# Kernel optimization log

Hardware: AMD Instinct MI355X
Metric: run time of the kernel (lower is better)

## Reference

```python
import jax, jax.numpy as jnp
import numpy as np

DEPTH = 9            # perfect binary tree depth (root=level 0, leaves=level DEPTH)
N_TREES = 128
H = 256              # h_size == x_size (ndata['h'] init uses x_size)
NPT = 2 ** (DEPTH + 1) - 1   # 1023 nodes per tree
N = N_TREES * NPT            # 130944 total nodes


def _levels():
    """Static per-level (node, left-child, right-child) global index arrays."""
    base = np.arange(N_TREES, dtype=np.int64)[:, None] * NPT
    out = []
    for l in range(DEPTH + 1):
        loc = np.arange(2 ** l - 1, 2 ** (l + 1) - 1, dtype=np.int64)
        nodes = (base + loc[None, :]).reshape(-1)
        if l < DEPTH:
            cl = (base + (2 * loc + 1)[None, :]).reshape(-1)
            cr = (base + (2 * loc + 2)[None, :]).reshape(-1)
        else:
            cl = cr = None
        out.append((jnp.asarray(nodes),
                    None if cl is None else jnp.asarray(cl),
                    None if cr is None else jnp.asarray(cr)))
    return out


def setup_inputs() -> dict:
    key = jax.random.key(0)
    ks = jax.random.split(key, 10)
    s = lambda d: 1.0 / np.sqrt(d)
    return {
        "wordid": jax.random.randint(ks[0], (N,), 0, 32000),
        "mask":   jax.random.randint(ks[1], (N,), 0, 2),
        "emb":    jax.random.normal(ks[2], (32000, H), jnp.float32) * 0.02,
        "W_iou":  jax.random.normal(ks[3], (H, 3 * H), jnp.float32) * s(H),
        "U_iou":  jax.random.normal(ks[4], (2 * H, 3 * H), jnp.float32) * s(2 * H),
        "U_f_w":  jax.random.normal(ks[5], (2 * H, 2 * H), jnp.float32) * s(2 * H),
        "U_f_b":  jax.random.normal(ks[6], (2 * H,), jnp.float32) * 0.01,
        "b_iou":  jax.random.normal(ks[7], (3 * H,), jnp.float32) * 0.01,
        "lin_w":  jax.random.normal(ks[8], (H, 4), jnp.float32) * s(H),
        "lin_b":  jax.random.normal(ks[9], (4,), jnp.float32) * 0.01,
    }


def _apply_node(iou, b_iou, c_in, mh_in):
    i, o, u = jnp.split(iou + b_iou, 3, axis=1)
    i, o, u = jax.nn.sigmoid(i), jax.nn.sigmoid(o), jnp.tanh(u)
    c = i * u + c_in
    h = o * jnp.tanh(c)
    return h, c, jnp.maximum(h, mh_in)


def reference(wordid, mask, emb, W_iou, U_iou, U_f_w, U_f_b, b_iou, lin_w, lin_b):
    levels = _levels()
    x = emb[wordid * mask]                                  # [N, H]
    iou0 = (x @ W_iou) * mask[:, None].astype(x.dtype)      # leaf/pre-set iou [N, 3H]

    h = jnp.zeros((N, H), x.dtype)
    c = jnp.zeros((N, H), x.dtype)
    mh = jnp.zeros((N, H), x.dtype)

    # leaves: no incoming messages -> apply with preset iou, c=0, max_h=0
    li, _, _ = levels[DEPTH]
    hh, cc, mm = _apply_node(iou0[li], b_iou, 0.0, 0.0)
    h, c, mh = h.at[li].set(hh), c.at[li].set(cc), mh.at[li].set(mm)

    # internal levels, bottom-up (DGL prop_nodes_topo)
    for l in range(DEPTH - 1, -1, -1):
        ni, cl, cr = levels[l]
        h_cat = jnp.concatenate([h[cl], h[cr]], axis=1)     # [M, 2H]
        f = jax.nn.sigmoid(h_cat @ U_f_w + U_f_b)           # [M, 2H]
        fl, fr = jnp.split(f, 2, axis=1)
        c_red = fl * c[cl] + fr * c[cr]
        mh_red = jnp.maximum(mh[cl], mh[cr])
        iou = h_cat @ U_iou                                  # overwrites preset iou
        hh, cc, mm = _apply_node(iou, b_iou, c_red, mh_red)
        h, c, mh = h.at[ni].set(hh), c.at[ni].set(cc), mh.at[ni].set(mm)

    return (h + mh) @ lin_w + lin_b                         # logits [N, num_classes]
```

## Files before the change

kernel.cpp:

```cpp
#include <hip/hip_runtime.h>
#include <hip/hip_bf16.h>


#define NTREES 128
#define NPT    1023
#define HS     256

typedef __hip_bfloat16 bf16;
typedef unsigned short us8 __attribute__((ext_vector_type(8)));
typedef short bf16x8 __attribute__((ext_vector_type(8)));
typedef float f32x4 __attribute__((ext_vector_type(4)));

typedef __attribute__((address_space(1))) const void gvoid;
typedef __attribute__((address_space(3))) void svoid;
#define GLD16(gp, lp) \
    __builtin_amdgcn_global_load_lds((gvoid*)(gp), (svoid*)(lp), 16, 0, 0)

__device__ __forceinline__ float bits2f(unsigned short b) {
    return __uint_as_float(((unsigned)b) << 16);
}
__device__ __forceinline__ float ld_bf(const bf16* p) {
    return bits2f(*reinterpret_cast<const unsigned short*>(p));
}
__device__ __forceinline__ unsigned short f2bits(float x) {
    bf16 h = __float2bfloat16(x);
    return *reinterpret_cast<unsigned short*>(&h);
}
__device__ __forceinline__ float sigm(float x) { return 1.0f / (1.0f + expf(-x)); }

#define WT_ELEMS (768 * 256)
#define UT_ELEMS (1280 * 512)

__global__ __launch_bounds__(256) void prep_w(
    const float* __restrict__ W_iou, const float* __restrict__ U_f_w,
    const float* __restrict__ U_iou, bf16* __restrict__ Wt, bf16* __restrict__ Ut)
{
    const int i = blockIdx.x * 256 + threadIdx.x;
    if (i < WT_ELEMS) {
        const int n = i >> 8, k = i & 255;
        Wt[i] = __float2bfloat16(W_iou[k * 768 + n]);
    } else if (i < WT_ELEMS + UT_ELEMS) {
        const int j = i - WT_ELEMS;
        const int n = j >> 9, k = j & 511;
        const float v = (n < 512) ? U_f_w[k * 512 + n] : U_iou[k * 768 + (n - 512)];
        Ut[j] = __float2bfloat16(v);
    }
}

__global__ __launch_bounds__(256) void leaf_gemm_mfma(
    const int* __restrict__ wordid, const int* __restrict__ mask,
    const float* __restrict__ emb, const bf16* __restrict__ Wt,
    bf16* __restrict__ lin, const int g0)
{
    __shared__ __align__(16) short a_s[128 * 32];
    __shared__ __align__(16) short b_s[128 * 32];
    const int t    = threadIdx.x;
    const int bm0  = blockIdx.x * 128;
    const int bn0  = blockIdx.y * 128;
    const int lane = t & 63, wave = t >> 6;

    const int arow_lo = t >> 2;
    const int k8t     = (t & 3) * 8;
    const float* aptr[2];
    int amask[2];
    #pragma unroll
    for (int p = 0; p < 2; ++p) {
        const int row  = p * 64 + arow_lo;
        const int gr   = g0 + bm0 + row;
        const int tree = gr >> 9, idx = gr & 511;
        const int node = tree * NPT + 511 + idx;
        amask[p] = mask[node];
        aptr[p]  = emb + (long)wordid[node] * HS + k8t;
    }

    const int l4a = lane >> 2;
    const int k8  = (lane & 3) * 8;
    const bf16* bSrc[2];
    #pragma unroll
    for (int q = 0; q < 2; ++q) {
        const int n = wave * 2 + q;
        bSrc[q] = Wt + (long)(bn0 + n * 16 + l4a) * 256 + k8;
    }

    const int wr = wave >> 1, wc = wave & 1;
    const int fr = lane & 15, l4 = lane >> 4;

    f32x4 acc[4][4];
    #pragma unroll
    for (int i = 0; i < 4; ++i)
        #pragma unroll
        for (int j = 0; j < 4; ++j) acc[i][j] = (f32x4){0.f, 0.f, 0.f, 0.f};

    for (int kt = 0; kt < 256; kt += 32) {
        __syncthreads();
        #pragma unroll
        for (int q = 0; q < 2; ++q)
            GLD16(bSrc[q] + kt, &b_s[(wave * 2 + q) * 512]);
        #pragma unroll
        for (int p = 0; p < 2; ++p) {
            short tmp[8];
            if (amask[p]) {
                const float4 v0 = *(const float4*)(aptr[p] + kt);
                const float4 v1 = *(const float4*)(aptr[p] + kt + 4);
                tmp[0] = (short)f2bits(v0.x); tmp[1] = (short)f2bits(v0.y);
                tmp[2] = (short)f2bits(v0.z); tmp[3] = (short)f2bits(v0.w);
                tmp[4] = (short)f2bits(v1.x); tmp[5] = (short)f2bits(v1.y);
                tmp[6] = (short)f2bits(v1.z); tmp[7] = (short)f2bits(v1.w);
            } else {
                #pragma unroll
                for (int q = 0; q < 8; ++q) tmp[q] = 0;
            }
            *(us8*)&a_s[p * 2048 + t * 8] = *(us8*)&tmp[0];
        }
        __syncthreads();
        bf16x8 af[4], bg[4];
        #pragma unroll
        for (int i = 0; i < 4; ++i)
            af[i] = *(const bf16x8*)&a_s[(wr * 64 + i * 16 + fr) * 32 + l4 * 8];
        #pragma unroll
        for (int j = 0; j < 4; ++j)
            bg[j] = *(const bf16x8*)&b_s[(wc * 64 + j * 16 + fr) * 32 + l4 * 8];
        #pragma unroll
        for (int i = 0; i < 4; ++i)
            #pragma unroll
            for (int j = 0; j < 4; ++j)
                acc[i][j] = __builtin_amdgcn_mfma_f32_16x16x32_bf16(
                    af[i], bg[j], acc[i][j], 0, 0, 0);
    }
    #pragma unroll
    for (int i = 0; i < 4; ++i) {
        const int row0 = bm0 + wr * 64 + i * 16 + l4 * 4;
        #pragma unroll
        for (int j = 0; j < 4; ++j) {
            const int col = bn0 + wc * 64 + j * 16 + fr;
            #pragma unroll
            for (int q = 0; q < 4; ++q)
                lin[(long)(row0 + q) * 768 + col] = __float2bfloat16(acc[i][j][q]);
        }
    }
}

__global__ __launch_bounds__(256) void level_gemm_mfma(
    const bf16* __restrict__ h_child, const bf16* __restrict__ Ut,
    bf16* __restrict__ lin, const int lvl, const int p0, const int M)
{
    __shared__ __align__(16) short a_s[128 * 32];
    __shared__ __align__(16) short b_s[128 * 32];
    const int t    = threadIdx.x;
    const int bm0  = blockIdx.x * 128;
    const int bn0  = blockIdx.y * 128;
    const int lane = t & 63, wave = t >> 6;

    const int l4a = lane >> 2;
    const int k8  = (lane & 3) * 8;
    const bf16* aSrc[2];
    const bf16* bSrc[2];
    #pragma unroll
    for (int q = 0; q < 2; ++q) {
        const int n = wave * 2 + q;
        int p = p0 + bm0 + n * 16 + l4a;
        if (p >= M) p = M - 1;
        const int tl  = p >> lvl;
        const int idx = p & ((1 << lvl) - 1);
        const int cls = tl * (2 << lvl) + 2 * idx;
        aSrc[q] = h_child + (long)cls * HS + k8;
        bSrc[q] = Ut + (long)(bn0 + n * 16 + l4a) * 512 + k8;
    }

    const int wr = wave >> 1, wc = wave & 1;
    const int fr = lane & 15, l4 = lane >> 4;

    f32x4 acc[4][4];
    #pragma unroll
    for (int i = 0; i < 4; ++i)
        #pragma unroll
        for (int j = 0; j < 4; ++j) acc[i][j] = (f32x4){0.f, 0.f, 0.f, 0.f};

    for (int kt = 0; kt < 512; kt += 32) {
        __syncthreads();
        #pragma unroll
        for (int q = 0; q < 2; ++q) {
            GLD16(aSrc[q] + kt, &a_s[(wave * 2 + q) * 512]);
            GLD16(bSrc[q] + kt, &b_s[(wave * 2 + q) * 512]);
        }
        __syncthreads();
        bf16x8 af[4], bg[4];
        #pragma unroll
        for (int i = 0; i < 4; ++i)
            af[i] = *(const bf16x8*)&a_s[(wr * 64 + i * 16 + fr) * 32 + l4 * 8];
        #pragma unroll
        for (int j = 0; j < 4; ++j)
            bg[j] = *(const bf16x8*)&b_s[(wc * 64 + j * 16 + fr) * 32 + l4 * 8];
        #pragma unroll
        for (int i = 0; i < 4; ++i)
            #pragma unroll
            for (int j = 0; j < 4; ++j)
                acc[i][j] = __builtin_amdgcn_mfma_f32_16x16x32_bf16(
                    af[i], bg[j], acc[i][j], 0, 0, 0);
    }
    #pragma unroll
    for (int i = 0; i < 4; ++i) {
        const int row0 = bm0 + wr * 64 + i * 16 + l4 * 4;
        #pragma unroll
        for (int j = 0; j < 4; ++j) {
            const int col = bn0 + wc * 64 + j * 16 + fr;
            #pragma unroll
            for (int q = 0; q < 4; ++q) {
                const int rr = row0 + q;
                if (p0 + rr < M)
                    lin[(long)rr * 1280 + col] = __float2bfloat16(acc[i][j][q]);
            }
        }
    }
}

__device__ __forceinline__ void logits_reduce(
    float s, const float* __restrict__ lin_w, const float* __restrict__ lin_b,
    float* __restrict__ outp, int j)
{
    const float4 w = *(const float4*)(lin_w + j * 4);
    float p0 = s * w.x, p1 = s * w.y, p2 = s * w.z, p3 = s * w.w;
    #pragma unroll
    for (int off = 32; off > 0; off >>= 1) {
        p0 += __shfl_down(p0, off);
        p1 += __shfl_down(p1, off);
        p2 += __shfl_down(p2, off);
        p3 += __shfl_down(p3, off);
    }
    __shared__ float red[4][4];
    const int w_id = j >> 6, lane = j & 63;
    if (lane == 0) { red[w_id][0] = p0; red[w_id][1] = p1; red[w_id][2] = p2; red[w_id][3] = p3; }
    __syncthreads();
    if (j < 4) {
        outp[j] = red[0][j] + red[1][j] + red[2][j] + red[3][j] + lin_b[j];
    }
}

__global__ __launch_bounds__(256) void leaf_epi(
    const int* __restrict__ mask, const bf16* __restrict__ lin,
    const float* __restrict__ b_iou,
    const float* __restrict__ lin_w, const float* __restrict__ lin_b,
    bf16* __restrict__ h_s, bf16* __restrict__ c_s, bf16* __restrict__ mh_s,
    float* __restrict__ out, const int g0, const int s0)
{
    const int rc   = blockIdx.x;
    const int gr   = g0 + rc;
    const int tree = gr >> 9, idx = gr & 511;
    const int node = tree * NPT + 511 + idx;
    const int j    = threadIdx.x;
    const int m    = mask[node];
    const bf16* lr = lin + (long)rc * 768;

    const float pi = (m ? ld_bf(lr + j)       : 0.0f) + b_iou[j];
    const float po = (m ? ld_bf(lr + 256 + j) : 0.0f) + b_iou[256 + j];
    const float pu = (m ? ld_bf(lr + 512 + j) : 0.0f) + b_iou[512 + j];
    const float iv = sigm(pi), ov = sigm(po), uv = tanhf(pu);
    const float cv  = iv * uv;
    const float hv  = ov * tanhf(cv);
    const float mhv = fmaxf(hv, 0.0f);

    const long o = (long)(s0 + rc) * HS + j;
    h_s[o]  = __float2bfloat16(hv);
    c_s[o]  = __float2bfloat16(cv);
    mh_s[o] = __float2bfloat16(mhv);

    logits_reduce(hv + mhv, lin_w, lin_b, out + (long)node * 4, j);
}

__global__ __launch_bounds__(256) void level_epi(
    const bf16* __restrict__ lin,
    const float* __restrict__ b_iou, const float* __restrict__ U_f_b,
    const float* __restrict__ lin_w, const float* __restrict__ lin_b,
    const bf16* __restrict__ c_c, const bf16* __restrict__ mh_c,
    bf16* __restrict__ h_p, bf16* __restrict__ c_p, bf16* __restrict__ mh_p,
    float* __restrict__ out, const int lvl, const int p0, const int tree0)
{
    const int rc   = blockIdx.x;
    const int p    = p0 + rc;
    const int tl   = p >> lvl, idx = p & ((1 << lvl) - 1);
    const int node = (tree0 + tl) * NPT + (1 << lvl) - 1 + idx;
    const int cls  = tl * (2 << lvl) + 2 * idx;
    const int j    = threadIdx.x;
    const bf16* lr = lin + (long)rc * 1280;

    const float fl = sigm(ld_bf(lr + j)       + U_f_b[j]);
    const float fr = sigm(ld_bf(lr + 256 + j) + U_f_b[256 + j]);
    const float pi = ld_bf(lr + 512 + j)  + b_iou[j];
    const float po = ld_bf(lr + 768 + j)  + b_iou[256 + j];
    const float pu = ld_bf(lr + 1024 + j) + b_iou[512 + j];

    const float ccl = ld_bf(c_c  + (long)cls * HS + j);
    const float ccr = ld_bf(c_c  + (long)(cls + 1) * HS + j);
    const float mhl = ld_bf(mh_c + (long)cls * HS + j);
    const float mhr = ld_bf(mh_c + (long)(cls + 1) * HS + j);

    const float c_red  = fl * ccl + fr * ccr;
    const float mh_red = fmaxf(mhl, mhr);

    const float iv = sigm(pi), ov = sigm(po), uv = tanhf(pu);
    const float cv  = iv * uv + c_red;
    const float hv  = ov * tanhf(cv);
    const float mhv = fmaxf(hv, mh_red);

    const long o = (long)p * HS + j;
    h_p[o]  = __float2bfloat16(hv);
    c_p[o]  = __float2bfloat16(cv);
    mh_p[o] = __float2bfloat16(mhv);

    logits_reduce(hv + mhv, lin_w, lin_b, out + (long)node * 4, j);
}

extern "C" void kernel_launch(void* const* d_in, const int* in_sizes, int n_in,
                              void* d_out, int out_size, void* d_ws, size_t ws_size,
                              hipStream_t stream) {
    const int*   wordid = (const int*)d_in[0];
    const int*   mask   = (const int*)d_in[1];
    const float* emb    = (const float*)d_in[2];
    const float* W_iou  = (const float*)d_in[3];
    const float* U_iou  = (const float*)d_in[4];
    const float* U_f_w  = (const float*)d_in[5];
    const float* U_f_b  = (const float*)d_in[6];
    const float* b_iou  = (const float*)d_in[7];
    const float* lin_w  = (const float*)d_in[8];
    const float* lin_b  = (const float*)d_in[9];
    float* out = (float*)d_out;

    const size_t wElems   = (size_t)WT_ELEMS + UT_ELEMS;
    const size_t ws_elems = ws_size / 2;
    auto baseElems = [&](int T) -> size_t {
        return wElems + (size_t)T * 589824;
    };
    const size_t minLin = 128 * 1280;
    int T = 8;
    const int cands[4] = {128, 64, 32, 16};
    for (int ci = 0; ci < 4; ++ci) {
        if (baseElems(cands[ci]) + minLin <= ws_elems) { T = cands[ci]; break; }
    }
    const size_t linCap = ws_elems - baseElems(T);

    bf16* Wt = (bf16*)d_ws;
    bf16* Ut = Wt + WT_ELEMS;
    const size_t aR = (size_t)T * 512 * HS;
    const size_t bR = (size_t)T * 256 * HS;
    bf16* hA  = Ut  + UT_ELEMS;
    bf16* cA  = hA  + aR;
    bf16* mhA = cA  + aR;
    bf16* hB  = mhA + aR;
    bf16* cB  = hB  + bR;
    bf16* mhB = cB  + bR;
    bf16* lin = mhB + bR;

    prep_w<<<(int)((wElems + 255) / 256), 256, 0, stream>>>(
        W_iou, U_f_w, U_iou, Wt, Ut);

    int CRl = (int)((linCap / 768) & ~(size_t)127);
    int CRv = (int)((linCap / 1280) & ~(size_t)127);
    if (CRl < 128) CRl = 128;
    if (CRv < 128) CRv = 128;

    for (int tree0 = 0; tree0 < NTREES; tree0 += T) {
        const int Ml = T * 512;
        for (int r0 = 0; r0 < Ml; r0 += CRl) {
            const int rows = (Ml - r0) < CRl ? (Ml - r0) : CRl;
            const int g0   = tree0 * 512 + r0;
            leaf_gemm_mfma<<<dim3(rows / 128, 6), 256, 0, stream>>>(
                wordid, mask, emb, Wt, lin, g0);
            leaf_epi<<<rows, 256, 0, stream>>>(
                mask, lin, b_iou, lin_w, lin_b, hA, cA, mhA, out, g0, r0);
        }
        bool childIsA = true;
        for (int l = 8; l >= 0; --l) {
            bf16 *hc, *cc, *mc, *hp, *cp, *mp;
            if (childIsA) { hc = hA; cc = cA; mc = mhA; hp = hB; cp = cB; mp = mhB; }
            else          { hc = hB; cc = cB; mc = mhB; hp = hA; cp = cA; mp = mhA; }
            const int M = T << l;
            for (int p0 = 0; p0 < M; p0 += CRv) {
                const int rows = (M - p0) < CRv ? (M - p0) : CRv;
                level_gemm_mfma<<<dim3((rows + 127) / 128, 10), 256, 0, stream>>>(
                    hc, Ut, lin, l, p0, M);
                level_epi<<<rows, 256, 0, stream>>>(
                    lin, b_iou, U_f_b, lin_w, lin_b, cc, mc, hp, cp, mp,
                    out, l, p0, tree0);
            }
            childIsA = !childIsA;
        }
    }
}
```

Baseline: 522.9 us.

## Map one wavefront per node row in epilogues with vectorized loads and fast math

The leaf and level epilogue kernels now assign one 64-lane wavefront per row, not one 256-thread block. Each lane handles four columns with 8-byte vector loads and stores, and the logits reduction becomes a wave-level xor shuffle, dropping the shared-memory stage and the block barrier. Sigmoid and tanh are rewritten with fast exp and hardware reciprocal. The aim is fewer blocks, wider memory accesses and no synchronisation, at some cost in transcendental accuracy.

Result: faster. 461.1 us (-11.8%).

```diff
diff --git a/kernel.cpp b/kernel.cpp
--- a/kernel.cpp
+++ b/kernel.cpp
@@ -8,6 +8,7 @@
 
 typedef __hip_bfloat16 bf16;
 typedef unsigned short us8 __attribute__((ext_vector_type(8)));
+typedef unsigned short us4 __attribute__((ext_vector_type(4)));
 typedef short bf16x8 __attribute__((ext_vector_type(8)));
 typedef float f32x4 __attribute__((ext_vector_type(4)));
 
@@ -19,14 +20,16 @@
 __device__ __forceinline__ float bits2f(unsigned short b) {
     return __uint_as_float(((unsigned)b) << 16);
 }
-__device__ __forceinline__ float ld_bf(const bf16* p) {
-    return bits2f(*reinterpret_cast<const unsigned short*>(p));
-}
 __device__ __forceinline__ unsigned short f2bits(float x) {
     bf16 h = __float2bfloat16(x);
     return *reinterpret_cast<unsigned short*>(&h);
 }
-__device__ __forceinline__ float sigm(float x) { return 1.0f / (1.0f + expf(-x)); }
+__device__ __forceinline__ float fsigm(float x) {
+    return __builtin_amdgcn_rcpf(1.0f + __expf(-x));
+}
+__device__ __forceinline__ float ftanh(float x) {
+    return 1.0f - 2.0f * __builtin_amdgcn_rcpf(1.0f + __expf(2.0f * x));
+}
 
 #define WT_ELEMS (768 * 256)
 #define UT_ELEMS (1280 * 512)
@@ -214,57 +217,62 @@
     }
 }
 
-__device__ __forceinline__ void logits_reduce(
-    float s, const float* __restrict__ lin_w, const float* __restrict__ lin_b,
-    float* __restrict__ outp, int j)
-{
-    const float4 w = *(const float4*)(lin_w + j * 4);
-    float p0 = s * w.x, p1 = s * w.y, p2 = s * w.z, p3 = s * w.w;
-    #pragma unroll
-    for (int off = 32; off > 0; off >>= 1) {
-        p0 += __shfl_down(p0, off);
-        p1 += __shfl_down(p1, off);
-        p2 += __shfl_down(p2, off);
-        p3 += __shfl_down(p3, off);
-    }
-    __shared__ float red[4][4];
-    const int w_id = j >> 6, lane = j & 63;
-    if (lane == 0) { red[w_id][0] = p0; red[w_id][1] = p1; red[w_id][2] = p2; red[w_id][3] = p3; }
-    __syncthreads();
-    if (j < 4) {
-        outp[j] = red[0][j] + red[1][j] + red[2][j] + red[3][j] + lin_b[j];
-    }
-}
-
 __global__ __launch_bounds__(256) void leaf_epi(
     const int* __restrict__ mask, const bf16* __restrict__ lin,
     const float* __restrict__ b_iou,
     const float* __restrict__ lin_w, const float* __restrict__ lin_b,
     bf16* __restrict__ h_s, bf16* __restrict__ c_s, bf16* __restrict__ mh_s,
-    float* __restrict__ out, const int g0, const int s0)
+    float* __restrict__ out, const int g0, const int s0, const int rows)
 {
-    const int rc   = blockIdx.x;
+    const int wave = threadIdx.x >> 6, lane = threadIdx.x & 63;
+    const int rc   = blockIdx.x * 4 + wave;
+    if (rc >= rows) return;
     const int gr   = g0 + rc;
     const int tree = gr >> 9, idx = gr & 511;
     const int node = tree * NPT + 511 + idx;
-    const int j    = threadIdx.x;
-    const int m    = mask[node];
-    const bf16* lr = lin + (long)rc * 768;
-
-    const float pi = (m ? ld_bf(lr + j)       : 0.0f) + b_iou[j];
-    const float po = (m ? ld_bf(lr + 256 + j) : 0.0f) + b_iou[256 + j];
-    const float pu = (m ? ld_bf(lr + 512 + j) : 0.0f) + b_iou[512 + j];
-    const float iv = sigm(pi), ov = sigm(po), uv = tanhf(pu);
-    const float cv  = iv * uv;
-    const float hv  = ov * tanhf(cv);
-    const float mhv = fmaxf(hv, 0.0f);
-
-    const long o = (long)(s0 + rc) * HS + j;
-    h_s[o]  = __float2bfloat16(hv);
-    c_s[o]  = __float2bfloat16(cv);
-    mh_s[o] = __float2bfloat16(mhv);
-
-    logits_reduce(hv + mhv, lin_w, lin_b, out + (long)node * 4, j);
+    const float msk = mask[node] ? 1.0f : 0.0f;
+    const int j0   = lane * 4;
+
+    const bf16* lr = lin + (long)rc * 768 + j0;
+    const us4 vi = *(const us4*)(lr);
+    const us4 vo = *(const us4*)(lr + 256);
+    const us4 vu = *(const us4*)(lr + 512);
+    const float4 bi = *(const float4*)(b_iou + j0);
+    const float4 bo = *(const float4*)(b_iou + 256 + j0);
+    const float4 bu = *(const float4*)(b_iou + 512 + j0);
+
+    us4 sh, sc, sm;
+    float p0 = 0.f, p1 = 0.f, p2 = 0.f, p3 = 0.f;
+    #pragma unroll
+    for (int q = 0; q < 4; ++q) {
+        const float pi = msk * bits2f(vi[q]) + ((const float*)&bi)[q];
+        const float po = msk * bits2f(vo[q]) + ((const float*)&bo)[q];
+        const float pu = msk * bits2f(vu[q]) + ((const float*)&bu)[q];
+        const float iv = fsigm(pi), ov = fsigm(po), uv = ftanh(pu);
+        const float cv  = iv * uv;
+        const float hv  = ov * ftanh(cv);
+        const float mhv = fmaxf(hv, 0.0f);
+        sh[q] = f2bits(hv); sc[q] = f2bits(cv); sm[q] = f2bits(mhv);
+        const float s = hv + mhv;
+        const float4 w = *(const float4*)(lin_w + (j0 + q) * 4);
+        p0 += s * w.x; p1 += s * w.y; p2 += s * w.z; p3 += s * w.w;
+    }
+    const long o = (long)(s0 + rc) * HS + j0;
+    *(us4*)(h_s + o)  = sh;
+    *(us4*)(c_s + o)  = sc;
+    *(us4*)(mh_s + o) = sm;
+
+    #pragma unroll
+    for (int m = 1; m < 64; m <<= 1) {
+        p0 += __shfl_xor(p0, m); p1 += __shfl_xor(p1, m);
+        p2 += __shfl_xor(p2, m); p3 += __shfl_xor(p3, m);
+    }
+    if (lane == 0) {
+        float4 r;
+        r.x = p0 + lin_b[0]; r.y = p1 + lin_b[1];
+        r.z = p2 + lin_b[2]; r.w = p3 + lin_b[3];
+        *(float4*)(out + (long)node * 4) = r;
+    }
 }
 
 __global__ __launch_bounds__(256) void level_epi(
@@ -273,41 +281,70 @@
     const float* __restrict__ lin_w, const float* __restrict__ lin_b,
     const bf16* __restrict__ c_c, const bf16* __restrict__ mh_c,
     bf16* __restrict__ h_p, bf16* __restrict__ c_p, bf16* __restrict__ mh_p,
-    float* __restrict__ out, const int lvl, const int p0, const int tree0)
+    float* __restrict__ out, const int lvl, const int p0r, const int tree0,
+    const int rows)
 {
-    const int rc   = blockIdx.x;
-    const int p    = p0 + rc;
+    const int wave = threadIdx.x >> 6, lane = threadIdx.x & 63;
+    const int rc   = blockIdx.x * 4 + wave;
+    if (rc >= rows) return;
+    const int p    = p0r + rc;
     const int tl   = p >> lvl, idx = p & ((1 << lvl) - 1);
     const int node = (tree0 + tl) * NPT + (1 << lvl) - 1 + idx;
     const int cls  = tl * (2 << lvl) + 2 * idx;
-    const int j    = threadIdx.x;
-    const bf16* lr = lin + (long)rc * 1280;
-
-    const float fl = sigm(ld_bf(lr + j)       + U_f_b[j]);
-    const float fr = sigm(ld_bf(lr + 256 + j) + U_f_b[256 + j]);
-    const float pi = ld_bf(lr + 512 + j)  + b_iou[j];
-    const float po = ld_bf(lr + 768 + j)  + b_iou[256 + j];
-    const float pu = ld_bf(lr + 1024 + j) + b_iou[512 + j];
-
-    const float ccl = ld_bf(c_c  + (long)cls * HS + j);
-    const float ccr = ld_bf(c_c  + (long)(cls + 1) * HS + j);
-    const float mhl = ld_bf(mh_c + (long)cls * HS + j);
-    const float mhr = ld_bf(mh_c + (long)(cls + 1) * HS + j);
-
-    const float c_red  = fl * ccl + fr * ccr;
-    const float mh_red = fmaxf(mhl, mhr);
-
-    const float iv = sigm(pi), ov = sigm(po), uv = tanhf(pu);
-    const float cv  = iv * uv + c_red;
-    const float hv  = ov * tanhf(cv);
-    const float mhv = fmaxf(hv, mh_red);
-
-    const long o = (long)p * HS + j;
-    h_p[o]  = __float2bfloat16(hv);
-    c_p[o]  = __float2bfloat16(cv);
-    mh_p[o] = __float2bfloat16(mhv);
-
-    logits_reduce(hv + mhv, lin_w, lin_b, out + (long)node * 4, j);
+    const int j0   = lane * 4;
+
+    const bf16* lr = lin + (long)rc * 1280 + j0;
+    const us4 vfl = *(const us4*)(lr);
+    const us4 vfr = *(const us4*)(lr + 256);
+    const us4 vi  = *(const us4*)(lr + 512);
+    const us4 vo  = *(const us4*)(lr + 768);
+    const us4 vu  = *(const us4*)(lr + 1024);
+    const us4 vcl = *(const us4*)(c_c  + (long)cls * HS + j0);
+    const us4 vcr = *(const us4*)(c_c  + (long)(cls + 1) * HS + j0);
+    const us4 vml = *(const us4*)(mh_c + (long)cls * HS + j0);
+    const us4 vmr = *(const us4*)(mh_c + (long)(cls + 1) * HS + j0);
+    const float4 ufl = *(const float4*)(U_f_b + j0);
+    const float4 ufr = *(const float4*)(U_f_b + 256 + j0);
+    const float4 bi  = *(const float4*)(b_iou + j0);
+    const float4 bo  = *(const float4*)(b_iou + 256 + j0);
+    const float4 bu  = *(const float4*)(b_iou + 512 + j0);
+
+    us4 sh, sc, sm;
+    float p0 = 0.f, p1 = 0.f, p2 = 0.f, p3 = 0.f;
+    #pragma unroll
+    for (int q = 0; q < 4; ++q) {
+        const float fl = fsigm(bits2f(vfl[q]) + ((const float*)&ufl)[q]);
+        const float fr = fsigm(bits2f(vfr[q]) + ((const float*)&ufr)[q]);
+        const float pi = bits2f(vi[q]) + ((const float*)&bi)[q];
+        const float po = bits2f(vo[q]) + ((const float*)&bo)[q];
+        const float pu = bits2f(vu[q]) + ((const float*)&bu)[q];
+        const float c_red  = fl * bits2f(vcl[q]) + fr * bits2f(vcr[q]);
+        const float mh_red = fmaxf(bits2f(vml[q]), bits2f(vmr[q]));
+        const float iv = fsigm(pi), ov = fsigm(po), uv = ftanh(pu);
+        const float cv  = iv * uv + c_red;
+        const float hv  = ov * ftanh(cv);
+        const float mhv = fmaxf(hv, mh_red);
+        sh[q] = f2bits(hv); sc[q] = f2bits(cv); sm[q] = f2bits(mhv);
+        const float s = hv + mhv;
+        const float4 w = *(const float4*)(lin_w + (j0 + q) * 4);
+        p0 += s * w.x; p1 += s * w.y; p2 += s * w.z; p3 += s * w.w;
+    }
+    const long o = (long)p * HS + j0;
+    *(us4*)(h_p + o)  = sh;
+    *(us4*)(c_p + o)  = sc;
+    *(us4*)(mh_p + o) = sm;
+
+    #pragma unroll
+    for (int m = 1; m < 64; m <<= 1) {
+        p0 += __shfl_xor(p0, m); p1 += __shfl_xor(p1, m);
+        p2 += __shfl_xor(p2, m); p3 += __shfl_xor(p3, m);
+    }
+    if (lane == 0) {
+        float4 r;
+        r.x = p0 + lin_b[0]; r.y = p1 + lin_b[1];
+        r.z = p2 + lin_b[2]; r.w = p3 + lin_b[3];
+        *(float4*)(out + (long)node * 4) = r;
+    }
 }
 
 extern "C" void kernel_launch(void* const* d_in, const int* in_sizes, int n_in,
@@ -365,8 +402,8 @@
             const int g0   = tree0 * 512 + r0;
             leaf_gemm_mfma<<<dim3(rows / 128, 6), 256, 0, stream>>>(
                 wordid, mask, emb, Wt, lin, g0);
-            leaf_epi<<<rows, 256, 0, stream>>>(
-                mask, lin, b_iou, lin_w, lin_b, hA, cA, mhA, out, g0, r0);
+            leaf_epi<<<(rows + 3) / 4, 256, 0, stream>>>(
+                mask, lin, b_iou, lin_w, lin_b, hA, cA, mhA, out, g0, r0, rows);
         }
         bool childIsA = true;
         for (int l = 8; l >= 0; --l) {
@@ -378,9 +415,9 @@
                 const int rows = (M - p0) < CRv ? (M - p0) : CRv;
                 level_gemm_mfma<<<dim3((rows + 127) / 128, 10), 256, 0, stream>>>(
                     hc, Ut, lin, l, p0, M);
-                level_epi<<<rows, 256, 0, stream>>>(
+                level_epi<<<(rows + 3) / 4, 256, 0, stream>>>(
                     lin, b_iou, U_f_b, lin_w, lin_b, cc, mc, hp, cp, mp,
-                    out, l, p0, tree0);
+                    out, l, p0, tree0, rows);
             }
             childIsA = !childIsA;
         }
```

## Fuse gate epilogues into GEMMs with gate-interleaved column tiles, defer logits

Applied to the files above, without the earlier changes.

The leaf and level GEMM kernels now tile output columns so that each block computes all gates (i/o/u, plus fl/fr for levels) for a 32-wide slice of hidden units. The LSTM cell update is applied directly in the GEMM epilogue, which removes the bf16 round trip through the intermediate lin buffer and the separate per-row epilogue kernels. The per-node logits reduction moves to a single final kernel that reads a stored bf16 h+mh buffer covering all nodes. Sigmoid and tanh switch to fast exp/rcp forms. The changes add workspace for the full node buffer, lower precision from bf16 storage of h+mh before the final linear layer, and more accumulator registers per thread.

After: 453.6 us. 13.2% less time.

```diff
diff --git a/kernel.cpp b/kernel.cpp
--- a/kernel.cpp
+++ b/kernel.cpp
@@ -5,9 +5,11 @@
 #define NTREES 128
 #define NPT    1023
 #define HS     256
+#define NNODES (NTREES * NPT)
 
 typedef __hip_bfloat16 bf16;
 typedef unsigned short us8 __attribute__((ext_vector_type(8)));
+typedef unsigned short us4 __attribute__((ext_vector_type(4)));
 typedef short bf16x8 __attribute__((ext_vector_type(8)));
 typedef float f32x4 __attribute__((ext_vector_type(4)));
 
@@ -26,7 +28,12 @@
     bf16 h = __float2bfloat16(x);
     return *reinterpret_cast<unsigned short*>(&h);
 }
-__device__ __forceinline__ float sigm(float x) { return 1.0f / (1.0f + expf(-x)); }
+__device__ __forceinline__ float fsigm(float x) {
+    return __builtin_amdgcn_rcpf(1.0f + __expf(-x));
+}
+__device__ __forceinline__ float ftanh(float x) {
+    return 1.0f - 2.0f * __builtin_amdgcn_rcpf(1.0f + __expf(2.0f * x));
+}
 
 #define WT_ELEMS (768 * 256)
 #define UT_ELEMS (1280 * 512)
@@ -47,55 +54,58 @@
     }
 }
 
-__global__ __launch_bounds__(256) void leaf_gemm_mfma(
+__global__ __launch_bounds__(256) void leaf_fused(
     const int* __restrict__ wordid, const int* __restrict__ mask,
     const float* __restrict__ emb, const bf16* __restrict__ Wt,
-    bf16* __restrict__ lin, const int g0)
+    const float* __restrict__ b_iou,
+    bf16* __restrict__ h_s, bf16* __restrict__ c_s, bf16* __restrict__ mh_s,
+    bf16* __restrict__ s_full, const int tree0)
 {
     __shared__ __align__(16) short a_s[128 * 32];
-    __shared__ __align__(16) short b_s[128 * 32];
+    __shared__ __align__(16) short b_s[96 * 32];
     const int t    = threadIdx.x;
     const int bm0  = blockIdx.x * 128;
-    const int bn0  = blockIdx.y * 128;
+    const int c0   = blockIdx.y * 32;
     const int lane = t & 63, wave = t >> 6;
 
-    const int arow_lo = t >> 2;
-    const int k8t     = (t & 3) * 8;
+    const int k8t = (t & 3) * 8;
     const float* aptr[2];
     int amask[2];
     #pragma unroll
     for (int p = 0; p < 2; ++p) {
-        const int row  = p * 64 + arow_lo;
-        const int gr   = g0 + bm0 + row;
-        const int tree = gr >> 9, idx = gr & 511;
-        const int node = tree * NPT + 511 + idx;
+        const int row  = p * 64 + (t >> 2);
+        const int gr   = tree0 * 512 + bm0 + row;
+        const int node = (gr >> 9) * NPT + 511 + (gr & 511);
         amask[p] = mask[node];
         aptr[p]  = emb + (long)wordid[node] * HS + k8t;
     }
 
-    const int l4a = lane >> 2;
-    const int k8  = (lane & 3) * 8;
+    const int l4a = lane >> 2, k8 = (lane & 3) * 8;
+    const int bCnt = (wave < 3) ? 2 : 0;
+    const int bStart = wave * 2;
     const bf16* bSrc[2];
     #pragma unroll
     for (int q = 0; q < 2; ++q) {
-        const int n = wave * 2 + q;
-        bSrc[q] = Wt + (long)(bn0 + n * 16 + l4a) * 256 + k8;
+        int rb = (bStart + q) * 16 + l4a;
+        if (rb > 95) rb = 95;
+        const int g = rb >> 5, jl = rb & 31;
+        bSrc[q] = Wt + (long)(g * 256 + c0 + jl) * 256 + k8;
     }
 
     const int wr = wave >> 1, wc = wave & 1;
     const int fr = lane & 15, l4 = lane >> 4;
 
-    f32x4 acc[4][4];
+    f32x4 acc[4][3];
     #pragma unroll
     for (int i = 0; i < 4; ++i)
         #pragma unroll
-        for (int j = 0; j < 4; ++j) acc[i][j] = (f32x4){0.f, 0.f, 0.f, 0.f};
+        for (int g = 0; g < 3; ++g) acc[i][g] = (f32x4){0.f, 0.f, 0.f, 0.f};
 
     for (int kt = 0; kt < 256; kt += 32) {
         __syncthreads();
         #pragma unroll
         for (int q = 0; q < 2; ++q)
-            GLD16(bSrc[q] + kt, &b_s[(wave * 2 + q) * 512]);
+            if (q < bCnt) GLD16(bSrc[q] + kt, &b_s[(bStart + q) * 512]);
         #pragma unroll
         for (int p = 0; p < 2; ++p) {
             short tmp[8];
@@ -113,201 +123,176 @@
             *(us8*)&a_s[p * 2048 + t * 8] = *(us8*)&tmp[0];
         }
         __syncthreads();
-        bf16x8 af[4], bg[4];
+        bf16x8 af[4], bg[3];
         #pragma unroll
         for (int i = 0; i < 4; ++i)
             af[i] = *(const bf16x8*)&a_s[(wr * 64 + i * 16 + fr) * 32 + l4 * 8];
         #pragma unroll
-        for (int j = 0; j < 4; ++j)
-            bg[j] = *(const bf16x8*)&b_s[(wc * 64 + j * 16 + fr) * 32 + l4 * 8];
+        for (int g = 0; g < 3; ++g)
+            bg[g] = *(const bf16x8*)&b_s[(g * 32 + wc * 16 + fr) * 32 + l4 * 8];
         #pragma unroll
         for (int i = 0; i < 4; ++i)
             #pragma unroll
-            for (int j = 0; j < 4; ++j)
-                acc[i][j] = __builtin_amdgcn_mfma_f32_16x16x32_bf16(
-                    af[i], bg[j], acc[i][j], 0, 0, 0);
-    }
+            for (int g = 0; g < 3; ++g)
+                acc[i][g] = __builtin_amdgcn_mfma_f32_16x16x32_bf16(
+                    af[i], bg[g], acc[i][g], 0, 0, 0);
+    }
+
+    const int j  = c0 + wc * 16 + fr;
+    const float bi = b_iou[j], bo = b_iou[256 + j], bu = b_iou[512 + j];
     #pragma unroll
     for (int i = 0; i < 4; ++i) {
-        const int row0 = bm0 + wr * 64 + i * 16 + l4 * 4;
-        #pragma unroll
-        for (int j = 0; j < 4; ++j) {
-            const int col = bn0 + wc * 64 + j * 16 + fr;
-            #pragma unroll
-            for (int q = 0; q < 4; ++q)
-                lin[(long)(row0 + q) * 768 + col] = __float2bfloat16(acc[i][j][q]);
+        #pragma unroll
+        for (int q = 0; q < 4; ++q) {
+            const int r    = bm0 + wr * 64 + i * 16 + l4 * 4 + q;
+            const int gr   = tree0 * 512 + r;
+            const int node = (gr >> 9) * NPT + 511 + (gr & 511);
+            const float iv = fsigm(acc[i][0][q] + bi);
+            const float ov = fsigm(acc[i][1][q] + bo);
+            const float uv = ftanh(acc[i][2][q] + bu);
+            const float cv  = iv * uv;
+            const float hv  = ov * ftanh(cv);
+            const float mhv = fmaxf(hv, 0.0f);
+            const long o = (long)r * HS + j;
+            h_s[o]  = __float2bfloat16(hv);
+            c_s[o]  = __float2bfloat16(cv);
+            mh_s[o] = __float2bfloat16(mhv);
+            s_full[(long)node * HS + j] = __float2bfloat16(hv + mhv);
         }
     }
 }
 
-__global__ __launch_bounds__(256) void level_gemm_mfma(
-    const bf16* __restrict__ h_child, const bf16* __restrict__ Ut,
-    bf16* __restrict__ lin, const int lvl, const int p0, const int M)
+__global__ __launch_bounds__(256) void level_fused(
+    const bf16* __restrict__ h_child, const bf16* __restrict__ c_c,
+    const bf16* __restrict__ mh_c, const bf16* __restrict__ Ut,
+    const float* __restrict__ U_f_b, const float* __restrict__ b_iou,
+    bf16* __restrict__ h_p, bf16* __restrict__ c_p, bf16* __restrict__ mh_p,
+    bf16* __restrict__ s_full, const int lvl, const int M, const int tree0)
 {
     __shared__ __align__(16) short a_s[128 * 32];
-    __shared__ __align__(16) short b_s[128 * 32];
+    __shared__ __align__(16) short b_s[160 * 32];
     const int t    = threadIdx.x;
     const int bm0  = blockIdx.x * 128;
-    const int bn0  = blockIdx.y * 128;
+    const int c0   = blockIdx.y * 32;
     const int lane = t & 63, wave = t >> 6;
 
-    const int l4a = lane >> 2;
-    const int k8  = (lane & 3) * 8;
+    const int l4a = lane >> 2, k8 = (lane & 3) * 8;
+
     const bf16* aSrc[2];
-    const bf16* bSrc[2];
     #pragma unroll
     for (int q = 0; q < 2; ++q) {
-        const int n = wave * 2 + q;
-        int p = p0 + bm0 + n * 16 + l4a;
+        int p = bm0 + wave * 32 + q * 16 + l4a;
         if (p >= M) p = M - 1;
         const int tl  = p >> lvl;
         const int idx = p & ((1 << lvl) - 1);
         const int cls = tl * (2 << lvl) + 2 * idx;
         aSrc[q] = h_child + (long)cls * HS + k8;
-        bSrc[q] = Ut + (long)(bn0 + n * 16 + l4a) * 512 + k8;
+    }
+    const int bCnt   = (wave < 2) ? 3 : 2;
+    const int bStart = (wave < 2) ? wave * 3 : 6 + (wave - 2) * 2;
+    const bf16* bSrc[3];
+    #pragma unroll
+    for (int q = 0; q < 3; ++q) {
+        int rb = (bStart + q) * 16 + l4a;
+        if (rb > 159) rb = 159;
+        const int g = rb >> 5, jl = rb & 31;
+        bSrc[q] = Ut + (long)(g * 256 + c0 + jl) * 512 + k8;
     }
 
     const int wr = wave >> 1, wc = wave & 1;
     const int fr = lane & 15, l4 = lane >> 4;
 
-    f32x4 acc[4][4];
+    f32x4 acc[4][5];
     #pragma unroll
     for (int i = 0; i < 4; ++i)
         #pragma unroll
-        for (int j = 0; j < 4; ++j) acc[i][j] = (f32x4){0.f, 0.f, 0.f, 0.f};
+        for (int g = 0; g < 5; ++g) acc[i][g] = (f32x4){0.f, 0.f, 0.f, 0.f};
 
     for (int kt = 0; kt < 512; kt += 32) {
         __syncthreads();
         #pragma unroll
-        for (int q = 0; q < 2; ++q) {
+        for (int q = 0; q < 2; ++q)
             GLD16(aSrc[q] + kt, &a_s[(wave * 2 + q) * 512]);
-            GLD16(bSrc[q] + kt, &b_s[(wave * 2 + q) * 512]);
-        }
+        #pragma unroll
+        for (int q = 0; q < 3; ++q)
+            if (q < bCnt) GLD16(bSrc[q] + kt, &b_s[(bStart + q) * 512]);
         __syncthreads();
-        bf16x8 af[4], bg[4];
+        bf16x8 af[4], bg[5];
         #pragma unroll
         for (int i = 0; i < 4; ++i)
             af[i] = *(const bf16x8*)&a_s[(wr * 64 + i * 16 + fr) * 32 + l4 * 8];
         #pragma unroll
-        for (int j = 0; j < 4; ++j)
-            bg[j] = *(const bf16x8*)&b_s[(wc * 64 + j * 16 + fr) * 32 + l4 * 8];
+        for (int g = 0; g < 5; ++g)
+            bg[g] = *(const bf16x8*)&b_s[(g * 32 + wc * 16 + fr) * 32 + l4 * 8];
         #pragma unroll
         for (int i = 0; i < 4; ++i)
             #pragma unroll
-            for (int j = 0; j < 4; ++j)
-                acc[i][j] = __builtin_amdgcn_mfma_f32_16x16x32_bf16(
-                    af[i], bg[j], acc[i][j], 0, 0, 0);
-    }
+            for (int g = 0; g < 5; ++g)
+                acc[i][g] = __builtin_amdgcn_mfma_f32_16x16x32_bf16(
+                    af[i], bg[g], acc[i][g], 0, 0, 0);
+    }
+
+    const int j = c0 + wc * 16 + fr;
+    const float bfl = U_f_b[j], bfr = U_f_b[256 + j];
+    const float bi = b_iou[j], bo = b_iou[256 + j], bu = b_iou[512 + j];
     #pragma unroll
     for (int i = 0; i < 4; ++i) {
-        const int row0 = bm0 + wr * 64 + i * 16 + l4 * 4;
-        #pragma unroll
-        for (int j = 0; j < 4; ++j) {
-            const int col = bn0 + wc * 64 + j * 16 + fr;
-            #pragma unroll
-            for (int q = 0; q < 4; ++q) {
-                const int rr = row0 + q;
-                if (p0 + rr < M)
-                    lin[(long)rr * 1280 + col] = __float2bfloat16(acc[i][j][q]);
+        #pragma unroll
+        for (int q = 0; q < 4; ++q) {
+            const int p = bm0 + wr * 64 + i * 16 + l4 * 4 + q;
+            if (p < M) {
+                const int tl   = p >> lvl;
+                const int idx  = p & ((1 << lvl) - 1);
+                const int cls  = tl * (2 << lvl) + 2 * idx;
+                const int node = (tree0 + tl) * NPT + (1 << lvl) - 1 + idx;
+                const float flv = fsigm(acc[i][0][q] + bfl);
+                const float frv = fsigm(acc[i][1][q] + bfr);
+                const float iv  = fsigm(acc[i][2][q] + bi);
+                const float ov  = fsigm(acc[i][3][q] + bo);
+                const float uv  = ftanh(acc[i][4][q] + bu);
+                const float ccl = ld_bf(c_c  + (long)cls * HS + j);
+                const float ccr = ld_bf(c_c  + (long)(cls + 1) * HS + j);
+                const float mhl = ld_bf(mh_c + (long)cls * HS + j);
+                const float mhr = ld_bf(mh_c + (long)(cls + 1) * HS + j);
+                const float cv  = iv * uv + flv * ccl + frv * ccr;
+                const float hv  = ov * ftanh(cv);
+                const float mhv = fmaxf(hv, fmaxf(mhl, mhr));
+                const long o = (long)p * HS + j;
+                h_p[o]  = __float2bfloat16(hv);
+                c_p[o]  = __float2bfloat16(cv);
+                mh_p[o] = __float2bfloat16(mhv);
+                s_full[(long)node * HS + j] = __float2bfloat16(hv + mhv);
             }
         }
     }
 }
 
-__device__ __forceinline__ void logits_reduce(
-    float s, const float* __restrict__ lin_w, const float* __restrict__ lin_b,
-    float* __restrict__ outp, int j)
+__global__ __launch_bounds__(256) void logits_k(
+    const bf16* __restrict__ s_full, const float* __restrict__ lin_w,
+    const float* __restrict__ lin_b, float* __restrict__ out)
 {
-    const float4 w = *(const float4*)(lin_w + j * 4);
-    float p0 = s * w.x, p1 = s * w.y, p2 = s * w.z, p3 = s * w.w;
-    #pragma unroll
-    for (int off = 32; off > 0; off >>= 1) {
-        p0 += __shfl_down(p0, off);
-        p1 += __shfl_down(p1, off);
-        p2 += __shfl_down(p2, off);
-        p3 += __shfl_down(p3, off);
-    }
-    __shared__ float red[4][4];
-    const int w_id = j >> 6, lane = j & 63;
-    if (lane == 0) { red[w_id][0] = p0; red[w_id][1] = p1; red[w_id][2] = p2; red[w_id][3] = p3; }
-    __syncthreads();
-    if (j < 4) {
-        outp[j] = red[0][j] + red[1][j] + red[2][j] + red[3][j] + lin_b[j];
-    }
-}
-
-__global__ __launch_bounds__(256) void leaf_epi(
-    const int* __restrict__ mask, const bf16* __restrict__ lin,
-    const float* __restrict__ b_iou,
-    const float* __restrict__ lin_w, const float* __restrict__ lin_b,
-    bf16* __restrict__ h_s, bf16* __restrict__ c_s, bf16* __restrict__ mh_s,
-    float* __restrict__ out, const int g0, const int s0)
-{
-    const int rc   = blockIdx.x;
-    const int gr   = g0 + rc;
-    const int tree = gr >> 9, idx = gr & 511;
-    const int node = tree * NPT + 511 + idx;
-    const int j    = threadIdx.x;
-    const int m    = mask[node];
-    const bf16* lr = lin + (long)rc * 768;
-
-    const float pi = (m ? ld_bf(lr + j)       : 0.0f) + b_iou[j];
-    const float po = (m ? ld_bf(lr + 256 + j) : 0.0f) + b_iou[256 + j];
-    const float pu = (m ? ld_bf(lr + 512 + j) : 0.0f) + b_iou[512 + j];
-    const float iv = sigm(pi), ov = sigm(po), uv = tanhf(pu);
-    const float cv  = iv * uv;
-    const float hv  = ov * tanhf(cv);
-    const float mhv = fmaxf(hv, 0.0f);
-
-    const long o = (long)(s0 + rc) * HS + j;
-    h_s[o]  = __float2bfloat16(hv);
-    c_s[o]  = __float2bfloat16(cv);
-    mh_s[o] = __float2bfloat16(mhv);
-
-    logits_reduce(hv + mhv, lin_w, lin_b, out + (long)node * 4, j);
-}
-
-__global__ __launch_bounds__(256) void level_epi(
-    const bf16* __restrict__ lin,
-    const float* __restrict__ b_iou, const float* __restrict__ U_f_b,
-    const float* __restrict__ lin_w, const float* __restrict__ lin_b,
-    const bf16* __restrict__ c_c, const bf16* __restrict__ mh_c,
-    bf16* __restrict__ h_p, bf16* __restrict__ c_p, bf16* __restrict__ mh_p,
-    float* __restrict__ out, const int lvl, const int p0, const int tree0)
-{
-    const int rc   = blockIdx.x;
-    const int p    = p0 + rc;
-    const int tl   = p >> lvl, idx = p & ((1 << lvl) - 1);
-    const int node = (tree0 + tl) * NPT + (1 << lvl) - 1 + idx;
-    const int cls  = tl * (2 << lvl) + 2 * idx;
-    const int j    = threadIdx.x;
-    const bf16* lr = lin + (long)rc * 1280;
-
-    const float fl = sigm(ld_bf(lr + j)       + U_f_b[j]);
-    const float fr = sigm(ld_bf(lr + 256 + j) + U_f_b[256 + j]);
-    const float pi = ld_bf(lr + 512 + j)  + b_iou[j];
-    const float po = ld_bf(lr + 768 + j)  + b_iou[256 + j];
-    const float pu = ld_bf(lr + 1024 + j) + b_iou[512 + j];
-
-    const float ccl = ld_bf(c_c  + (long)cls * HS + j);
-    const float ccr = ld_bf(c_c  + (long)(cls + 1) * HS + j);
-    const float mhl = ld_bf(mh_c + (long)cls * HS + j);
-    const float mhr = ld_bf(mh_c + (long)(cls + 1) * HS + j);
-
-    const float c_red  = fl * ccl + fr * ccr;
-    const float mh_red = fmaxf(mhl, mhr);
-
-    const float iv = sigm(pi), ov = sigm(po), uv = tanhf(pu);
-    const float cv  = iv * uv + c_red;
-    const float hv  = ov * tanhf(cv);
-    const float mhv = fmaxf(hv, mh_red);
-
-    const long o = (long)p * HS + j;
-    h_p[o]  = __float2bfloat16(hv);
-    c_p[o]  = __float2bfloat16(cv);
-    mh_p[o] = __float2bfloat16(mhv);
-
-    logits_reduce(hv + mhv, lin_w, lin_b, out + (long)node * 4, j);
+    const int wave = threadIdx.x >> 6, lane = threadIdx.x & 63;
+    const int node = blockIdx.x * 4 + wave;
+    const int j0   = lane * 4;
+    const us4 v = *(const us4*)(s_full + (long)node * HS + j0);
+    float p0 = 0.f, p1 = 0.f, p2 = 0.f, p3 = 0.f;
+    #pragma unroll
+    for (int q = 0; q < 4; ++q) {
+        const float s  = bits2f(v[q]);
+        const float4 w = *(const float4*)(lin_w + (j0 + q) * 4);
+        p0 += s * w.x; p1 += s * w.y; p2 += s * w.z; p3 += s * w.w;
+    }
+    #pragma unroll
+    for (int m = 1; m < 64; m <<= 1) {
+        p0 += __shfl_xor(p0, m); p1 += __shfl_xor(p1, m);
+        p2 += __shfl_xor(p2, m); p3 += __shfl_xor(p3, m);
+    }
+    if (lane == 0) {
+        float4 r;
+        r.x = p0 + lin_b[0]; r.y = p1 + lin_b[1];
+        r.z = p2 + lin_b[2]; r.w = p3 + lin_b[3];
+        *(float4*)(out + (long)node * 4) = r;
+    }
 }
 
 extern "C" void kernel_launch(void* const* d_in, const int* in_sizes, int n_in,
@@ -325,64 +310,45 @@
     const float* lin_b  = (const float*)d_in[9];
     float* out = (float*)d_out;
 
-    const size_t wElems   = (size_t)WT_ELEMS + UT_ELEMS;
-    const size_t ws_elems = ws_size / 2;
-    auto baseElems = [&](int T) -> size_t {
-        return wElems + (size_t)T * 589824;
+    const size_t wElems = (size_t)WT_ELEMS + UT_ELEMS;
+    const size_t sElems = (size_t)NNODES * HS;
+    auto need = [&](int T) -> size_t {
+        return (wElems + sElems + (size_t)T * 589824) * 2;
     };
-    const size_t minLin = 128 * 1280;
     int T = 8;
     const int cands[4] = {128, 64, 32, 16};
     for (int ci = 0; ci < 4; ++ci) {
-        if (baseElems(cands[ci]) + minLin <= ws_elems) { T = cands[ci]; break; }
-    }
-    const size_t linCap = ws_elems - baseElems(T);
-
-    bf16* Wt = (bf16*)d_ws;
-    bf16* Ut = Wt + WT_ELEMS;
+        if (need(cands[ci]) <= ws_size) { T = cands[ci]; break; }
+    }
+
+    bf16* Wt     = (bf16*)d_ws;
+    bf16* Ut     = Wt + WT_ELEMS;
+    bf16* s_full = Ut + UT_ELEMS;
     const size_t aR = (size_t)T * 512 * HS;
     const size_t bR = (size_t)T * 256 * HS;
-    bf16* hA  = Ut  + UT_ELEMS;
+    bf16* hA  = s_full + sElems;
     bf16* cA  = hA  + aR;
     bf16* mhA = cA  + aR;
     bf16* hB  = mhA + aR;
     bf16* cB  = hB  + bR;
     bf16* mhB = cB  + bR;
-    bf16* lin = mhB + bR;
 
     prep_w<<<(int)((wElems + 255) / 256), 256, 0, stream>>>(
         W_iou, U_f_w, U_iou, Wt, Ut);
 
-    int CRl = (int)((linCap / 768) & ~(size_t)127);
-    int CRv = (int)((linCap / 1280) & ~(size_t)127);
-    if (CRl < 128) CRl = 128;
-    if (CRv < 128) CRv = 128;
-
     for (int tree0 = 0; tree0 < NTREES; tree0 += T) {
-        const int Ml = T * 512;
-        for (int r0 = 0; r0 < Ml; r0 += CRl) {
-            const int rows = (Ml - r0) < CRl ? (Ml - r0) : CRl;
-            const int g0   = tree0 * 512 + r0;
-            leaf_gemm_mfma<<<dim3(rows / 128, 6), 256, 0, stream>>>(
-                wordid, mask, emb, Wt, lin, g0);
-            leaf_epi<<<rows, 256, 0, stream>>>(
-                mask, lin, b_iou, lin_w, lin_b, hA, cA, mhA, out, g0, r0);
-        }
+        leaf_fused<<<dim3(T * 512 / 128, 8), 256, 0, stream>>>(
+            wordid, mask, emb, Wt, b_iou, hA, cA, mhA, s_full, tree0);
         bool childIsA = true;
         for (int l = 8; l >= 0; --l) {
             bf16 *hc, *cc, *mc, *hp, *cp, *mp;
             if (childIsA) { hc = hA; cc = cA; mc = mhA; hp = hB; cp = cB; mp = mhB; }
             else          { hc = hB; cc = cB; mc = mhB; hp = hA; cp = cA; mp = mhA; }
             const int M = T << l;
-            for (int p0 = 0; p0 < M; p0 += CRv) {
-                const int rows = (M - p0) < CRv ? (M - p0) : CRv;
-                level_gemm_mfma<<<dim3((rows + 127) / 128, 10), 256, 0, stream>>>(
-                    hc, Ut, lin, l, p0, M);
-                level_epi<<<rows, 256, 0, stream>>>(
-                    lin, b_iou, U_f_b, lin_w, lin_b, cc, mc, hp, cp, mp,
-                    out, l, p0, tree0);
-            }
+            level_fused<<<dim3((M + 127) / 128, 8), 256, 0, stream>>>(
+                hc, cc, mc, Ut, U_f_b, b_iou, hp, cp, mp, s_full, l, M, tree0);
             childIsA = !childIsA;
         }
     }
-}
+    logits_k<<<NNODES / 4, 256, 0, stream>>>(s_full, lin_w, lin_b, out);
+}
```
